# Performance work log

Measured on AMD Instinct MI355X. Metric: run time of the kernel, lower is better.

## Reference

```python
import jax, jax.numpy as jnp
import numpy as np

NUM_FEAT = 1024
NUM_GROUP = 16
DIM_K = NUM_FEAT // NUM_GROUP  # 64
FEAT_DIM = 64
WAVE_LENGTH = 1000.0


def position_embedding(box, ctx_box):
    # box: (M,4), ctx_box: (N,4) corner encoding -> (M*N, 64)
    xmin, ymin, xmax, ymax = jnp.split(box, 4, axis=1)            # (M,1) each
    bw = xmax - xmin + 1.0
    bh = ymax - ymin + 1.0
    cx = 0.5 * (xmin + xmax)
    cy = 0.5 * (ymin + ymax)
    cxmin, cymin, cxmax, cymax = jnp.split(ctx_box, 4, axis=1)    # (N,1) each
    cbw = cxmax - cxmin + 1.0
    cbh = cymax - cymin + 1.0
    ccx = 0.5 * (cxmin + cxmax)
    ccy = 0.5 * (cymin + cymax)
    dx = jnp.log(jnp.clip(jnp.abs((cx - ccx.T) / bw), 1e-3))      # (M,N)
    dy = jnp.log(jnp.clip(jnp.abs((cy - ccy.T) / bh), 1e-3))
    dw = jnp.log(cbw.T / bw)
    dh = jnp.log(cbh.T / bh)
    pos = jnp.stack((dx, dy, dw, dh), axis=2)                     # (M,N,4)
    feat_range = jnp.arange(FEAT_DIM // 8, dtype=jnp.float32)     # (8,)
    dim_mat = jnp.power(jnp.float32(WAVE_LENGTH), (8.0 / FEAT_DIM) * feat_range)
    div = (100.0 * pos)[..., None] / dim_mat                      # (M,N,4,8)
    emb = jnp.concatenate((jnp.sin(div), jnp.cos(div)), axis=3)   # (M,N,4,16)
    M, N = pos.shape[0], pos.shape[1]
    return emb.reshape(M * N, FEAT_DIM)


def setup_inputs() -> dict:
    key = jax.random.key(0)
    ks = jax.random.split(key, 12)
    M, N = 512, 1024

    def make_boxes(k, n):
        k1, k2 = jax.random.split(k)
        xy = jax.random.uniform(k1, (n, 2), dtype=jnp.float32) * 800.0
        wh = jax.random.uniform(k2, (n, 2), dtype=jnp.float32) * 200.0 + 1.0
        return jnp.concatenate([xy, xy + wh], axis=1)             # valid corners

    return {
        "feat": jax.random.normal(ks[0], (M, NUM_FEAT), dtype=jnp.float32),
        "ctx_feat": jax.random.normal(ks[1], (N, NUM_FEAT), dtype=jnp.float32),
        "box": make_boxes(ks[2], M),
        "ctx_box": make_boxes(ks[3], N),
        # torch Linear stores weight as (out, in); apply as x @ W.T + b
        "w_fc_gt": jax.random.normal(ks[4], (NUM_FEAT, 1024), dtype=jnp.float32) * 0.01,
        "b_fc_gt": jnp.zeros((NUM_FEAT,), dtype=jnp.float32),
        "w_fc_ctx": jax.random.normal(ks[5], (NUM_FEAT, 1024), dtype=jnp.float32) * 0.01,
        "b_fc_ctx": jnp.zeros((NUM_FEAT,), dtype=jnp.float32),
        "w_pos_gt": jax.random.normal(ks[6], (NUM_GROUP, FEAT_DIM), dtype=jnp.float32) * 0.01,
        "b_pos_gt": jnp.zeros((NUM_GROUP,), dtype=jnp.float32),
        "w_pos_ctx": jax.random.normal(ks[7], (NUM_GROUP, FEAT_DIM), dtype=jnp.float32) * 0.01,
        "b_pos_ctx": jnp.zeros((NUM_GROUP,), dtype=jnp.float32),
        # grouped 1x1 conv (16384 -> 1024, groups=16): per-group weight (64 out, 1024 in)
        "w_conv": jax.random.normal(ks[8], (NUM_GROUP, DIM_K, NUM_FEAT), dtype=jnp.float32) * 0.02,
        "b_conv": jnp.zeros((NUM_FEAT,), dtype=jnp.float32),
    }


def reference(feat, ctx_feat, box, ctx_box,
              w_fc_gt, b_fc_gt, w_fc_ctx, b_fc_ctx,
              w_pos_gt, b_pos_gt, w_pos_ctx, b_pos_ctx,
              w_conv, b_conv):
    M, N = feat.shape[0], ctx_feat.shape[0]
    # positional bias per group: (M*N,64) -relu-> linear -> (G,M,N)
    pe_gt = jax.nn.relu(position_embedding(box, ctx_box))
    pos_gt = (pe_gt @ w_pos_gt.T + b_pos_gt).T.reshape(NUM_GROUP, M, N)
    pe_ctx = jax.nn.relu(position_embedding(ctx_box, box))
    pos_ctx = (pe_ctx @ w_pos_ctx.T + b_pos_ctx).T.reshape(NUM_GROUP, N, M)
    # grouped projections
    q = (feat @ w_fc_gt.T + b_fc_gt).reshape(M, NUM_GROUP, DIM_K)
    k = (ctx_feat @ w_fc_ctx.T + b_fc_ctx).reshape(N, NUM_GROUP, DIM_K)
    scores = jnp.einsum('mgd,ngd->gmn', q, k) / np.float32(np.sqrt(DIM_K))  # (G,M,N)
    # gt <- ctx attention with log-position bias
    w1 = jax.nn.softmax(jnp.log(jnp.clip(pos_gt, 1e-6)) + scores, axis=-1)  # (G,M,N)
    att1 = jnp.einsum('gmn,nc->mgc', w1, ctx_feat)                          # (M,G,1024)
    out_gt = jnp.einsum('mgc,goc->mgo', att1, w_conv).reshape(M, NUM_FEAT) + b_conv
    # ctx <- gt attention (note: original module reuses gt_ctx_linear_out here)
    w2 = jax.nn.softmax(jnp.log(jnp.clip(pos_ctx, 1e-6)) + scores.transpose(0, 2, 1), axis=-1)  # (G,N,M)
    att2 = jnp.einsum('gnm,mc->ngc', w2, feat)                              # (N,G,1024)
    out_ctx = jnp.einsum('ngc,goc->ngo', att2, w_conv).reshape(N, NUM_FEAT) + b_conv
    return out_gt, out_ctx
```

## Files before the change

### kernel.cpp

```cpp
#include <hip/hip_runtime.h>
#include <math.h>


typedef __attribute__((ext_vector_type(8))) short short8;
typedef __attribute__((ext_vector_type(4))) float floatx4;
typedef __attribute__((ext_vector_type(4))) _Float16 half4;
typedef __attribute__((ext_vector_type(4))) unsigned uint4v;

__device__ inline unsigned short f32_bf16_rne(float x) {
    union { float f; unsigned u; } v; v.f = x;
    unsigned u = v.u;
    return (unsigned short)((u + 0x7fffu + ((u >> 16) & 1u)) >> 16);
}

__device__ inline unsigned fbits(float x) {
    union { float f; unsigned u; } v; v.f = x; return v.u;
}
__device__ inline float bitsf(unsigned u) {
    union { unsigned u; float f; } v; v.u = u; return v.f;
}
__device__ inline float h16f(unsigned short u) {
    union { unsigned short u; _Float16 h; } v; v.u = u; return (float)v.h;
}

__device__ __forceinline__ floatx4 mfma16(short8 a, short8 b, floatx4 c) {
    return __builtin_amdgcn_mfma_f32_16x16x32_bf16(a, b, c, 0, 0, 0);
}

__device__ __forceinline__ void gemm_tile_pack(
    const unsigned short* __restrict__ Ab, int lda,
    const unsigned short* __restrict__ Bb, int ldb, int K,
    unsigned short* __restrict__ out_base,
    const float* __restrict__ biasvec,
    unsigned short* As, unsigned short* Bs)
{
    const int tid = threadIdx.x;
    const int lr = tid >> 3;
    const int lk = (tid & 7) * 8;
    const int lane = tid & 63;
    const int wave = tid >> 6;
    const int qr = (wave >> 1) * 32;
    const int qc = (wave & 1) * 32;
    const int m = lane & 15;
    const int quad = lane >> 4;

    const unsigned short* Ap  = Ab + (long long)lr * lda + lk;
    const unsigned short* Ap2 = Ap + 32LL * lda;
    const unsigned short* Bp  = Bb + (long long)lr * ldb + lk;
    const unsigned short* Bp2 = Bp + 32LL * ldb;
    unsigned short* AsW  = As + lr * 72 + lk;
    unsigned short* AsW2 = As + (lr + 32) * 72 + lk;
    unsigned short* BsW  = Bs + lr * 72 + lk;
    unsigned short* BsW2 = Bs + (lr + 32) * 72 + lk;
    const unsigned short* a0p = As + (qr + m) * 72 + quad * 8;
    const unsigned short* b0p = Bs + (qc + m) * 72 + quad * 8;

    floatx4 acc00 = {0.f,0.f,0.f,0.f}, acc01 = {0.f,0.f,0.f,0.f};
    floatx4 acc10 = {0.f,0.f,0.f,0.f}, acc11 = {0.f,0.f,0.f,0.f};

    int4 pa0 = *(const int4*)Ap;
    int4 pa1 = *(const int4*)Ap2;
    int4 pb0 = *(const int4*)Bp;
    int4 pb1 = *(const int4*)Bp2;
    int4 qa0 = *(const int4*)(Ap + 64);
    int4 qa1 = *(const int4*)(Ap2 + 64);
    int4 qb0 = *(const int4*)(Bp + 64);
    int4 qb1 = *(const int4*)(Bp2 + 64);

    for (int k0 = 0; ; ) {
        __syncthreads();
        *(int4*)AsW  = pa0;
        *(int4*)AsW2 = pa1;
        *(int4*)BsW  = pb0;
        *(int4*)BsW2 = pb1;
        __syncthreads();
        pa0 = qa0; pa1 = qa1; pb0 = qb0; pb1 = qb1;
        const int kf = k0 + 128;
        if (kf < K) {
            qa0 = *(const int4*)(Ap + kf);
            qa1 = *(const int4*)(Ap2 + kf);
            qb0 = *(const int4*)(Bp + kf);
            qb1 = *(const int4*)(Bp2 + kf);
        }
        #pragma unroll
        for (int kk = 0; kk < 64; kk += 32) {
            short8 a0 = *(const short8*)(a0p + kk);
            short8 a1 = *(const short8*)(a0p + 16 * 72 + kk);
            short8 b0 = *(const short8*)(b0p + kk);
            short8 b1 = *(const short8*)(b0p + 16 * 72 + kk);
            acc00 = mfma16(a0, b0, acc00);
            acc01 = mfma16(a0, b1, acc01);
            acc10 = mfma16(a1, b0, acc10);
            acc11 = mfma16(a1, b1, acc11);
        }
        k0 += 64;
        if (k0 >= K) break;
    }

    float bias0 = 0.f, bias1 = 0.f;
    if (biasvec) { bias0 = biasvec[qc + m]; bias1 = biasvec[qc + 16 + m]; }

    __syncthreads();
    const floatx4 accs[2][2] = { {acc00, acc01}, {acc10, acc11} };
    #pragma unroll
    for (int i = 0; i < 2; ++i)
        #pragma unroll
        for (int r = 0; r < 4; ++r) {
            const int lrow = qr + i * 16 + quad * 4 + r;
            #pragma unroll
            for (int j = 0; j < 2; ++j) {
                const int lcol = qc + j * 16 + m;
                float val = accs[i][j][r] + (j ? bias1 : bias0);
                As[lrow * 72 + lcol] = f32_bf16_rne(val);
            }
        }
    __syncthreads();
    #pragma unroll
    for (int h = 0; h < 2; ++h) {
        const int f = h * 2048 + tid * 8;
        const int lanep = (f >> 3) & 63;
        const int part = (f >> 9) & 1;
        const int ploc = f >> 10;
        const int row = ploc * 16 + (lanep & 15);
        const int col = part * 32 + ((lanep >> 4) << 3);
        short8 v8 = *(const short8*)&As[row * 72 + col];
        *(short8*)(out_base + f) = v8;
    }
}

__global__ __launch_bounds__(256) void cast_kernel(
    const float* __restrict__ s0, unsigned short* __restrict__ d0,
    const float* __restrict__ s1, unsigned short* __restrict__ d1,
    const float* __restrict__ s2, unsigned short* __restrict__ d2,
    const float* __restrict__ s3, unsigned short* __restrict__ d3,
    const float* __restrict__ s4, unsigned short* __restrict__ d4)
{
    int bc = blockIdx.x;
    const float* s; unsigned short* d;
    if (bc < 512)       { s = s0; d = d0; }
    else if (bc < 1536) { s = s1; d = d1; bc -= 512; }
    else if (bc < 2560) { s = s2; d = d2; bc -= 1536; }
    else if (bc < 3584) { s = s3; d = d3; bc -= 2560; }
    else                { s = s4; d = d4; bc -= 3584; }
    const int idx = (bc * 256 + threadIdx.x) * 4;
    float4 v = *(const float4*)(s + idx);
    ushort4 o;
    o.x = f32_bf16_rne(v.x); o.y = f32_bf16_rne(v.y);
    o.z = f32_bf16_rne(v.z); o.w = f32_bf16_rne(v.w);
    *(ushort4*)(d + idx) = o;
}

__global__ __launch_bounds__(256) void posproj_kernel(
    const float* __restrict__ box, const float* __restrict__ ctx_box,
    const float* __restrict__ w_gt, const float* __restrict__ b_gt,
    const float* __restrict__ w_ctx, const float* __restrict__ b_ctx,
    _Float16* __restrict__ bias_gt, _Float16* __restrict__ bias_ctx,
    const unsigned short* __restrict__ in_bf, const unsigned short* __restrict__ wgt,
    const unsigned short* __restrict__ wctx,
    const float* __restrict__ bgt, const float* __restrict__ bctx,
    unsigned short* __restrict__ qk_pack,
    const unsigned short* __restrict__ wconv, unsigned short* __restrict__ vt_pack)
{
    __shared__ __align__(16) unsigned short smem[64 * 72 * 2];
    const int i = blockIdx.x;

    int pi;
    if (i < 4608) {
        const int k48 = i / 48;
        const int r48 = i - k48 * 48;
        if (r48 < 8) {
            const int j = r48;
            const int k = k48;
            const int g = j + 8 * (k & 1);
            const int rest = k >> 1;
            const int z = rest / 24;
            const int cc = rest - z * 24;
            unsigned short* As = smem;
            unsigned short* Bs = smem + 64 * 72;
            if (z == 0) {
                const int bm = cc * 64;
                const unsigned short* B = (bm < 512) ? wgt : wctx;
                const float* bias = (bm < 512) ? bgt : bctx;
                gemm_tile_pack(in_bf + (long long)bm * 1024, 1024,
                               B + (long long)g * 65536, 1024, 1024,
                               qk_pack + ((long long)g * 96 + cc * 4) * 1024,
                               bias + g * 64, As, Bs);
            } else {
                gemm_tile_pack(wconv + (long long)g * 65536, 1024,
                               in_bf + (long long)cc * 65536, 1024, 1024,
                               vt_pack + ((long long)g * 24 + cc) * 4096,
                               nullptr, As, Bs);
            }
            return;
        }
        pi = i - k48 * 8 - 8;
    } else {
        pi = i - 768;
    }

    const bool first = (pi < 2048);
    const long long blk = first ? pi : (pi - 2048);
    const float* boxA = first ? box : ctx_box;
    const float* boxB = first ? ctx_box : box;
    const float* w_pos = first ? w_gt : w_ctx;
    const float* b_pos = first ? b_gt : b_ctx;
    _Float16* out = first ? bias_gt : bias_ctx;
    const int shift = first ? 10 : 9;

    unsigned short* BsH = smem;
    unsigned short* BsL = smem + 16 * 72;
    float* posL = (float*)(smem + 32 * 72);
    _Float16* stg = (_Float16*)(posL + 4 * 68);

    const int tid = threadIdx.x;

    {
        const int g = tid >> 4;
        const int d = (tid & 15) * 4;
        float4 wv = *(const float4*)(w_pos + g * 64 + d);
        unsigned u0 = fbits(wv.x), u1 = fbits(wv.y);
        unsigned u2 = fbits(wv.z), u3 = fbits(wv.w);
        unsigned r0 = fbits(wv.x - bitsf(u0 & 0xFFFF0000u));
        unsigned r1 = fbits(wv.y - bitsf(u1 & 0xFFFF0000u));
        unsigned r2 = fbits(wv.z - bitsf(u2 & 0xFFFF0000u));
        unsigned r3 = fbits(wv.w - bitsf(u3 & 0xFFFF0000u));
        uint2 hv, lv;
        hv.x = (u0 >> 16) | (u1 & 0xFFFF0000u);
        hv.y = (u2 >> 16) | (u3 & 0xFFFF0000u);
        lv.x = (r0 >> 16) | (r1 & 0xFFFF0000u);
        lv.y = (r2 >> 16) | (r3 & 0xFFFF0000u);
        *(uint2*)&BsH[g * 72 + d] = hv;
        *(uint2*)&BsL[g * 72 + d] = lv;
    }
    __syncthreads();

    const int lane = tid & 63;
    const int w = tid >> 6;
    const int m = lane & 15;
    const int quad = lane >> 4;
    const bool qlow = (quad < 2);
    const float phase = (quad & 1) ? 1.57079632679f : 0.0f;
    const float bpv = b_pos[m];

    const unsigned short* bpH = &BsH[m * 72 + quad * 8];
    const unsigned short* bpL = &BsL[m * 72 + quad * 8];
    short8 bH0 = *(const short8*)bpH;
    short8 bH1 = *(const short8*)(bpH + 32);
    short8 bL0 = *(const short8*)bpL;
    short8 bL1 = *(const short8*)(bpL + 32);

    const float w100[8] = {100.f, 42.169650342f, 17.782794100f, 7.498942093f,
                           3.162277660f, 1.333521432f, 0.562341325f, 0.237137371f};
    const long long pbase = blk * 256;

    for (int it = 0; it < 4; ++it) {
        const long long pb = pbase + it * 64;

        {
            const int pl = tid & 63;
            const int p = tid >> 6;
            const long long pair = pb + pl;
            const int i2 = (int)(pair >> shift);
            const int j2 = (int)(pair & ((1 << shift) - 1));
            float4 ba = *(const float4*)(boxA + i2 * 4);
            float4 bb = *(const float4*)(boxB + j2 * 4);
            float posv;
            if (p == 0) {
                float r = __builtin_amdgcn_rcpf(ba.z - ba.x + 1.f);
                posv = __logf(fmaxf(fabsf((0.5f*(ba.x+ba.z) - 0.5f*(bb.x+bb.z)) * r), 1e-3f));
            } else if (p == 1) {
                float r = __builtin_amdgcn_rcpf(ba.w - ba.y + 1.f);
                posv = __logf(fmaxf(fabsf((0.5f*(ba.y+ba.w) - 0.5f*(bb.y+bb.w)) * r), 1e-3f));
            } else if (p == 2) {
                float r = __builtin_amdgcn_rcpf(ba.z - ba.x + 1.f);
                posv = __logf((bb.z - bb.x + 1.f) * r);
            } else {
                float r = __builtin_amdgcn_rcpf(ba.w - ba.y + 1.f);
                posv = __logf((bb.w - bb.y + 1.f) * r);
            }
            posL[p * 68 + pl] = posv;
        }
        __syncthreads();

        const int plB = w * 16 + m;
        const float pos_lo = posL[(qlow ? 0 : 1) * 68 + plB];
        const float pos_hi = posL[(qlow ? 2 : 3) * 68 + plB];

        unsigned hp0[4], lp0[4], hp1[4], lp1[4];
        #pragma unroll
        for (int fi = 0; fi < 4; ++fi) {
            float x0 = fmaxf(__sinf(fmaf(w100[2*fi],     pos_lo, phase)), 0.f);
            float x1 = fmaxf(__sinf(fmaf(w100[2*fi + 1], pos_lo, phase)), 0.f);
            unsigned u0 = fbits(x0), u1 = fbits(x1);
            unsigned r0 = fbits(x0 - bitsf(u0 & 0xFFFF0000u));
            unsigned r1 = fbits(x1 - bitsf(u1 & 0xFFFF0000u));
            hp0[fi] = (u0 >> 16) | (u1 & 0xFFFF0000u);
            lp0[fi] = (r0 >> 16) | (r1 & 0xFFFF0000u);
            float y0 = fmaxf(__sinf(fmaf(w100[2*fi],     pos_hi, phase)), 0.f);
            float y1 = fmaxf(__sinf(fmaf(w100[2*fi + 1], pos_hi, phase)), 0.f);
            unsigned v0 = fbits(y0), v1 = fbits(y1);
            unsigned s0r = fbits(y0 - bitsf(v0 & 0xFFFF0000u));
            unsigned s1r = fbits(y1 - bitsf(v1 & 0xFFFF0000u));
            hp1[fi] = (v0 >> 16) | (v1 & 0xFFFF0000u);
            lp1[fi] = (s0r >> 16) | (s1r & 0xFFFF0000u);
        }
        union { uint4v u; short8 s; } cH0, cL0, cH1, cL1;
        cH0.u = (uint4v){hp0[0], hp0[1], hp0[2], hp0[3]};
        cL0.u = (uint4v){lp0[0], lp0[1], lp0[2], lp0[3]};
        cH1.u = (uint4v){hp1[0], hp1[1], hp1[2], hp1[3]};
        cL1.u = (uint4v){lp1[0], lp1[1], lp1[2], lp1[3]};

        floatx4 acc = {0.f, 0.f, 0.f, 0.f};
        acc = mfma16(cH0.s, bH0, acc);
        acc = mfma16(cH1.s, bH1, acc);
        acc = mfma16(cH0.s, bL0, acc);
        acc = mfma16(cH1.s, bL1, acc);
        acc = mfma16(cL0.s, bH0, acc);
        acc = mfma16(cL1.s, bH1, acc);

        #pragma unroll
        for (int r = 0; r < 4; ++r)
            stg[m * 68 + w * 16 + quad * 4 + r] =
                (_Float16)fmaxf(acc[r] + bpv, 1e-6f);
        __syncthreads();

        const int g2 = tid >> 4, c16 = tid & 15;
        *(half4*)(out + (long long)g2 * 524288 + pb + c16 * 4) =
            *(const half4*)&stg[g2 * 68 + c16 * 4];
    }
}

template <int NC>
__device__ __forceinline__ void attn_body(
    int g, int bx,
    const unsigned short* __restrict__ qk, int pA, int pB0,
    const _Float16* __restrict__ bias,
    const unsigned short* __restrict__ vt, int cc0,
    const float* __restrict__ b_conv, float* __restrict__ outp,
    unsigned short* wpack, float* redB)
{
    constexpr int NCOL = NC * 64;
    constexpr int WS = NCOL + 8;
    constexpr int SHIFT = (NC == 16) ? 10 : 9;

    const int bm = bx * 16;
    const int tid = threadIdx.x;
    const int lane = tid & 63;
    const int w = tid >> 6;
    const int m = lane & 15;
    const int quad = lane >> 4;

    {
        const _Float16* bsrc = bias + (long long)g * 524288 + (long long)bm * NCOL;
        _Float16* bb = (_Float16*)wpack;
        #pragma unroll
        for (int i = 0; i < (16 * NCOL) / (256 * 8); ++i) {
            const int idx = (i * 256 + tid) * 8;
            const int row = idx >> SHIFT;
            const int col = idx & (NCOL - 1);
            *(int4*)(bb + row * WS + col) = *(const int4*)(bsrc + idx);
        }
    }

    const unsigned short* abase = qk + ((long long)(g * 96 + pA)) * 1024;
    short8 aq0 = *(const short8*)(abase + lane * 8);
    short8 aq1 = *(const short8*)(abase + 512 + lane * 8);

    const unsigned short* bptr = qk + ((long long)(g * 96 + pB0 + w)) * 1024 + lane * 8;
    short8 B0[2], B1[2];
    B0[0] = *(const short8*)bptr;
    B1[0] = *(const short8*)(bptr + 512);
    B0[1] = *(const short8*)(bptr + 4096);
    B1[1] = *(const short8*)(bptr + 4096 + 512);

    __syncthreads();

    float v[NC][4];
    #pragma unroll
    for (int c = 0; c < NC; ++c) {
        floatx4 acc = {0.f, 0.f, 0.f, 0.f};
        acc = mfma16(aq0, B0[c & 1], acc);
        acc = mfma16(aq1, B1[c & 1], acc);
        if (c + 2 < NC) {
            const unsigned short* nb = bptr + (long long)(c + 2) * 4096;
            B0[c & 1] = *(const short8*)nb;
            B1[c & 1] = *(const short8*)(nb + 512);
        }
        #pragma unroll
        for (int r = 0; r < 4; ++r)
            v[c][r] = acc[r];
    }

    const unsigned short* vptr = vt + ((long long)(g * 24 + cc0)) * 4096
                               + w * 1024 + lane * 8;
    short8 V0[2], V1[2];
    V0[0] = *(const short8*)vptr;
    V1[0] = *(const short8*)(vptr + 512);
    V0[1] = *(const short8*)(vptr + 4096);
    V1[1] = *(const short8*)(vptr + 4096 + 512);

    const int slot0 = (quad * 4) * WS + w * 16 + m;
    float rsum[4] = {0.f, 0.f, 0.f, 0.f};
    #pragma unroll
    for (int c = 0; c < NC; ++c)
        #pragma unroll
        for (int r = 0; r < 4; ++r) {
            const int a = slot0 + r * WS + c * 64;
            float p = h16f(wpack[a]);
            float e = exp2f(v[c][r] * 0.18033688f) * p;
            rsum[r] += e;
            wpack[a] = f32_bf16_rne(e);
        }
    #pragma unroll
    for (int r = 0; r < 4; ++r)
        #pragma unroll
        for (int off = 1; off < 16; off <<= 1)
            rsum[r] += __shfl_xor(rsum[r], off, 64);
    if (m == 0) {
        #pragma unroll
        for (int r = 0; r < 4; ++r) redB[w * 16 + quad * 4 + r] = rsum[r];
    }
    __syncthreads();

    float rinv[4];
    #pragma unroll
    for (int r = 0; r < 4; ++r)
        rinv[r] = 1.f / (redB[quad*4+r] + redB[16 + quad*4+r] +
                         redB[32 + quad*4+r] + redB[48 + quad*4+r]);

    floatx4 oacc = {0.f, 0.f, 0.f, 0.f};
    const unsigned short* awp = wpack + m * WS + quad * 8;
    #pragma unroll
    for (int kc = 0; kc < NC; ++kc) {
        short8 a0 = *(const short8*)(awp + kc * 64);
        short8 a1 = *(const short8*)(awp + kc * 64 + 32);
        oacc = mfma16(a0, V0[kc & 1], oacc);
        oacc = mfma16(a1, V1[kc & 1], oacc);
        if (kc + 2 < NC) {
            const unsigned short* nv = vptr + (long long)(kc + 2) * 4096;
            V0[kc & 1] = *(const short8*)nv;
            V1[kc & 1] = *(const short8*)(nv + 512);
        }
    }

    const int o = w * 16 + m;
    const float bc = b_conv[g * 64 + o];
    __syncthreads();
    float* ot = (float*)wpack;
    #pragma unroll
    for (int r = 0; r < 4; ++r)
        ot[(quad * 4 + r) * 68 + o] = fmaf(oacc[r], rinv[r], bc);
    __syncthreads();
    const int orow = tid >> 4, oc4 = (tid & 15) * 4;
    float4 ov = *(const float4*)&ot[orow * 68 + oc4];
    *(float4*)(outp + (long long)(bm + orow) * 1024 + g * 64 + oc4) = ov;
}

__global__ __launch_bounds__(256) void attn_out_kernel(
    const unsigned short* __restrict__ qk_pack,
    const _Float16* __restrict__ bias_gt, const _Float16* __restrict__ bias_ctx,
    const unsigned short* __restrict__ vt_pack, const float* __restrict__ b_conv,
    float* __restrict__ out_gt, float* __restrict__ out_ctx)
{
    __shared__ __align__(16) unsigned short wpack[16 * 1032];
    __shared__ float redB[64];

    const int bx = blockIdx.x;
    if (bx < 512) {
        const int g = bx & 15;
        const int rb = bx >> 4;
        attn_body<16>(g, rb, qk_pack, rb, 32,
                      bias_gt, vt_pack, 8, b_conv, out_gt,
                      wpack, redB);
    } else {
        const int b2 = bx - 512;
        const int g = b2 & 15;
        const int rb = b2 >> 4;
        attn_body<8>(g, rb, qk_pack, 32 + rb, 0,
                     bias_ctx, vt_pack, 0, b_conv, out_ctx,
                     wpack, redB);
    }
}

extern "C" void kernel_launch(void* const* d_in, const int* in_sizes, int n_in,
                              void* d_out, int out_size, void* d_ws, size_t ws_size,
                              hipStream_t stream)
{
    const float* feat     = (const float*)d_in[0];
    const float* ctx_feat = (const float*)d_in[1];
    const float* box      = (const float*)d_in[2];
    const float* ctx_box  = (const float*)d_in[3];
    const float* w_fc_gt  = (const float*)d_in[4];
    const float* b_fc_gt  = (const float*)d_in[5];
    const float* w_fc_ctx = (const float*)d_in[6];
    const float* b_fc_ctx = (const float*)d_in[7];
    const float* w_pos_gt = (const float*)d_in[8];
    const float* b_pos_gt = (const float*)d_in[9];
    const float* w_pos_ctx= (const float*)d_in[10];
    const float* b_pos_ctx= (const float*)d_in[11];
    const float* w_conv   = (const float*)d_in[12];
    const float* b_conv   = (const float*)d_in[13];

    float* ws = (float*)d_ws;
    unsigned short* in_bf   = (unsigned short*)ws;
    unsigned short* ctx_bf  = in_bf + 524288LL;
    unsigned short* qk_pack = in_bf + 1572864LL;
    _Float16* bias_gt  = (_Float16*)(ws + 1572864LL);
    _Float16* bias_ctx = (_Float16*)(ws + 5767168LL);
    unsigned short* wconv_bf = (unsigned short*)(ws + 9961472LL);
    unsigned short* vt_pack  = (unsigned short*)(ws + 10485760LL);
    unsigned short* wfcgt_bf = (unsigned short*)(ws + 11272192LL);
    unsigned short* wfcctx_bf= wfcgt_bf + 1048576LL;

    float* out_gt  = (float*)d_out;
    float* out_ctx = (float*)d_out + 524288LL;

    hipLaunchKernelGGL(cast_kernel, dim3(4608), dim3(256), 0, stream,
                       feat, in_bf,
                       ctx_feat, ctx_bf,
                       w_fc_gt, wfcgt_bf,
                       w_fc_ctx, wfcctx_bf,
                       w_conv, wconv_bf);

    hipLaunchKernelGGL(posproj_kernel, dim3(4864), dim3(256), 0, stream,
                       box, ctx_box, w_pos_gt, b_pos_gt, w_pos_ctx, b_pos_ctx,
                       bias_gt, bias_ctx,
                       in_bf, wfcgt_bf, wfcctx_bf, b_fc_gt, b_fc_ctx, qk_pack,
                       wconv_bf, vt_pack);

    hipLaunchKernelGGL(attn_out_kernel, dim3(1536), dim3(256), 0, stream,
                       qk_pack, bias_gt, bias_ctx, vt_pack, b_conv, out_gt, out_ctx);
}
```

Measured before the change: 147.6 us.

## Compute position features in registers and double attention rows per block

The position-projection kernel now computes each lane's position values directly from box coordinates, dropping the shared-memory staging and one barrier per iteration. Its output staging buffer is double-buffered across iterations. The attention kernel moves to 512-thread blocks covering 32 rows, with two row-groups of waves sharing the bias tile loads and V fragments. The exp/softmax weighting is fused into the score loop so the per-column scores no longer sit in a large register array. In exchange the blocks use more LDS and there are half as many of them, which may reduce occupancy.

Measured after the change: 147.4 us. Within noise of the previous version (-0.1%).

```diff
diff --git a/kernel.cpp b/kernel.cpp
--- a/kernel.cpp
+++ b/kernel.cpp
@@ -209,8 +209,7 @@
 
     unsigned short* BsH = smem;
     unsigned short* BsL = smem + 16 * 72;
-    float* posL = (float*)(smem + 32 * 72);
-    _Float16* stg = (_Float16*)(posL + 4 * 68);
+    _Float16* stg = (_Float16*)(smem + 32 * 72);
 
     const int tid = threadIdx.x;
 
@@ -241,6 +240,7 @@
     const bool qlow = (quad < 2);
     const float phase = (quad & 1) ? 1.57079632679f : 0.0f;
     const float bpv = b_pos[m];
+    const int plB = w * 16 + m;
 
     const unsigned short* bpH = &BsH[m * 72 + quad * 8];
     const unsigned short* bpL = &BsL[m * 72 + quad * 8];
@@ -256,35 +256,16 @@
     for (int it = 0; it < 4; ++it) {
         const long long pb = pbase + it * 64;
 
-        {
-            const int pl = tid & 63;
-            const int p = tid >> 6;
-            const long long pair = pb + pl;
-            const int i2 = (int)(pair >> shift);
-            const int j2 = (int)(pair & ((1 << shift) - 1));
-            float4 ba = *(const float4*)(boxA + i2 * 4);
-            float4 bb = *(const float4*)(boxB + j2 * 4);
-            float posv;
-            if (p == 0) {
-                float r = __builtin_amdgcn_rcpf(ba.z - ba.x + 1.f);
-                posv = __logf(fmaxf(fabsf((0.5f*(ba.x+ba.z) - 0.5f*(bb.x+bb.z)) * r), 1e-3f));
-            } else if (p == 1) {
-                float r = __builtin_amdgcn_rcpf(ba.w - ba.y + 1.f);
-                posv = __logf(fmaxf(fabsf((0.5f*(ba.y+ba.w) - 0.5f*(bb.y+bb.w)) * r), 1e-3f));
-            } else if (p == 2) {
-                float r = __builtin_amdgcn_rcpf(ba.z - ba.x + 1.f);
-                posv = __logf((bb.z - bb.x + 1.f) * r);
-            } else {
-                float r = __builtin_amdgcn_rcpf(ba.w - ba.y + 1.f);
-                posv = __logf((bb.w - bb.y + 1.f) * r);
-            }
-            posL[p * 68 + pl] = posv;
-        }
-        __syncthreads();
-
-        const int plB = w * 16 + m;
-        const float pos_lo = posL[(qlow ? 0 : 1) * 68 + plB];
-        const float pos_hi = posL[(qlow ? 2 : 3) * 68 + plB];
+        const int i2 = (int)(pb >> shift);
+        const int j2 = (int)(pb & ((1 << shift) - 1)) + plB;
+        float4 ba = *(const float4*)(boxA + i2 * 4);
+        float4 bb = *(const float4*)(boxB + j2 * 4);
+        const float a0 = qlow ? ba.x : ba.y, a1 = qlow ? ba.z : ba.w;
+        const float b0 = qlow ? bb.x : bb.y, b1 = qlow ? bb.z : bb.w;
+        const float rr = __builtin_amdgcn_rcpf(a1 - a0 + 1.f);
+        const float pos_lo =
+            __logf(fmaxf(fabsf((0.5f*(a0+a1) - 0.5f*(b0+b1)) * rr), 1e-3f));
+        const float pos_hi = __logf((b1 - b0 + 1.f) * rr);
 
         unsigned hp0[4], lp0[4], hp1[4], lp1[4];
         #pragma unroll
@@ -318,22 +299,23 @@
         acc = mfma16(cL0.s, bH0, acc);
         acc = mfma16(cL1.s, bH1, acc);
 
+        _Float16* s = stg + (it & 1) * 1088;
         #pragma unroll
         for (int r = 0; r < 4; ++r)
-            stg[m * 68 + w * 16 + quad * 4 + r] =
+            s[m * 68 + w * 16 + quad * 4 + r] =
                 (_Float16)fmaxf(acc[r] + bpv, 1e-6f);
         __syncthreads();
 
         const int g2 = tid >> 4, c16 = tid & 15;
         *(half4*)(out + (long long)g2 * 524288 + pb + c16 * 4) =
-            *(const half4*)&stg[g2 * 68 + c16 * 4];
+            *(const half4*)&s[g2 * 68 + c16 * 4];
     }
 }
 
 template <int NC>
 __device__ __forceinline__ void attn_body(
-    int g, int bx,
-    const unsigned short* __restrict__ qk, int pA, int pB0,
+    int g, int bm,
+    const unsigned short* __restrict__ qk, int pA0, int pB0,
     const _Float16* __restrict__ bias,
     const unsigned short* __restrict__ vt, int cc0,
     const float* __restrict__ b_conv, float* __restrict__ outp,
@@ -342,11 +324,13 @@
     constexpr int NCOL = NC * 64;
     constexpr int WS = NCOL + 8;
     constexpr int SHIFT = (NC == 16) ? 10 : 9;
-
-    const int bm = bx * 16;
+    constexpr int NSTG = (32 * NCOL) / (512 * 8);
+
     const int tid = threadIdx.x;
     const int lane = tid & 63;
     const int w = tid >> 6;
+    const int ws = w >> 2;
+    const int wq = w & 3;
     const int m = lane & 15;
     const int quad = lane >> 4;
 
@@ -354,19 +338,19 @@
         const _Float16* bsrc = bias + (long long)g * 524288 + (long long)bm * NCOL;
         _Float16* bb = (_Float16*)wpack;
         #pragma unroll
-        for (int i = 0; i < (16 * NCOL) / (256 * 8); ++i) {
-            const int idx = (i * 256 + tid) * 8;
+        for (int i = 0; i < NSTG; ++i) {
+            const int idx = (i * 512 + tid) * 8;
             const int row = idx >> SHIFT;
             const int col = idx & (NCOL - 1);
             *(int4*)(bb + row * WS + col) = *(const int4*)(bsrc + idx);
         }
     }
 
-    const unsigned short* abase = qk + ((long long)(g * 96 + pA)) * 1024;
+    const unsigned short* abase = qk + ((long long)(g * 96 + pA0 + ws)) * 1024;
     short8 aq0 = *(const short8*)(abase + lane * 8);
     short8 aq1 = *(const short8*)(abase + 512 + lane * 8);
 
-    const unsigned short* bptr = qk + ((long long)(g * 96 + pB0 + w)) * 1024 + lane * 8;
+    const unsigned short* bptr = qk + ((long long)(g * 96 + pB0 + wq)) * 1024 + lane * 8;
     short8 B0[2], B1[2];
     B0[0] = *(const short8*)bptr;
     B1[0] = *(const short8*)(bptr + 512);
@@ -375,7 +359,8 @@
 
     __syncthreads();
 
-    float v[NC][4];
+    const int slot0 = (ws * 16 + quad * 4) * WS + wq * 16 + m;
+    float rsum[4] = {0.f, 0.f, 0.f, 0.f};
     #pragma unroll
     for (int c = 0; c < NC; ++c) {
         floatx4 acc = {0.f, 0.f, 0.f, 0.f};
@@ -387,30 +372,23 @@
             B1[c & 1] = *(const short8*)(nb + 512);
         }
         #pragma unroll
-        for (int r = 0; r < 4; ++r)
-            v[c][r] = acc[r];
+        for (int r = 0; r < 4; ++r) {
+            const int a = slot0 + r * WS + c * 64;
+            float p = h16f(wpack[a]);
+            float e = exp2f(acc[r] * 0.18033688f) * p;
+            rsum[r] += e;
+            wpack[a] = f32_bf16_rne(e);
+        }
     }
 
     const unsigned short* vptr = vt + ((long long)(g * 24 + cc0)) * 4096
-                               + w * 1024 + lane * 8;
+                               + wq * 1024 + lane * 8;
     short8 V0[2], V1[2];
     V0[0] = *(const short8*)vptr;
     V1[0] = *(const short8*)(vptr + 512);
     V0[1] = *(const short8*)(vptr + 4096);
     V1[1] = *(const short8*)(vptr + 4096 + 512);
 
-    const int slot0 = (quad * 4) * WS + w * 16 + m;
-    float rsum[4] = {0.f, 0.f, 0.f, 0.f};
-    #pragma unroll
-    for (int c = 0; c < NC; ++c)
-        #pragma unroll
-        for (int r = 0; r < 4; ++r) {
-            const int a = slot0 + r * WS + c * 64;
-            float p = h16f(wpack[a]);
-            float e = exp2f(v[c][r] * 0.18033688f) * p;
-            rsum[r] += e;
-            wpack[a] = f32_bf16_rne(e);
-        }
     #pragma unroll
     for (int r = 0; r < 4; ++r)
         #pragma unroll
@@ -425,11 +403,11 @@
     float rinv[4];
     #pragma unroll
     for (int r = 0; r < 4; ++r)
-        rinv[r] = 1.f / (redB[quad*4+r] + redB[16 + quad*4+r] +
-                         redB[32 + quad*4+r] + redB[48 + quad*4+r]);
+        rinv[r] = 1.f / (redB[ws*64 + quad*4+r] + redB[ws*64 + 16 + quad*4+r] +
+                         redB[ws*64 + 32 + quad*4+r] + redB[ws*64 + 48 + quad*4+r]);
 
     floatx4 oacc = {0.f, 0.f, 0.f, 0.f};
-    const unsigned short* awp = wpack + m * WS + quad * 8;
+    const unsigned short* awp = wpack + (ws * 16 + m) * WS + quad * 8;
     #pragma unroll
     for (int kc = 0; kc < NC; ++kc) {
         short8 a0 = *(const short8*)(awp + kc * 64);
@@ -443,40 +421,40 @@
         }
     }
 
-    const int o = w * 16 + m;
+    const int o = wq * 16 + m;
     const float bc = b_conv[g * 64 + o];
     __syncthreads();
     float* ot = (float*)wpack;
     #pragma unroll
     for (int r = 0; r < 4; ++r)
-        ot[(quad * 4 + r) * 68 + o] = fmaf(oacc[r], rinv[r], bc);
+        ot[(ws * 16 + quad * 4 + r) * 68 + o] = fmaf(oacc[r], rinv[r], bc);
     __syncthreads();
     const int orow = tid >> 4, oc4 = (tid & 15) * 4;
     float4 ov = *(const float4*)&ot[orow * 68 + oc4];
     *(float4*)(outp + (long long)(bm + orow) * 1024 + g * 64 + oc4) = ov;
 }
 
-__global__ __launch_bounds__(256) void attn_out_kernel(
+__global__ __launch_bounds__(512) void attn_out_kernel(
     const unsigned short* __restrict__ qk_pack,
     const _Float16* __restrict__ bias_gt, const _Float16* __restrict__ bias_ctx,
     const unsigned short* __restrict__ vt_pack, const float* __restrict__ b_conv,
     float* __restrict__ out_gt, float* __restrict__ out_ctx)
 {
-    __shared__ __align__(16) unsigned short wpack[16 * 1032];
-    __shared__ float redB[64];
+    __shared__ __align__(16) unsigned short wpack[32 * 1032];
+    __shared__ float redB[128];
 
     const int bx = blockIdx.x;
-    if (bx < 512) {
+    if (bx < 256) {
         const int g = bx & 15;
         const int rb = bx >> 4;
-        attn_body<16>(g, rb, qk_pack, rb, 32,
+        attn_body<16>(g, rb * 32, qk_pack, 2 * rb, 32,
                       bias_gt, vt_pack, 8, b_conv, out_gt,
                       wpack, redB);
     } else {
-        const int b2 = bx - 512;
+        const int b2 = bx - 256;
         const int g = b2 & 15;
         const int rb = b2 >> 4;
-        attn_body<8>(g, rb, qk_pack, 32 + rb, 0,
+        attn_body<8>(g, rb * 32, qk_pack, 32 + 2 * rb, 0,
                      bias_ctx, vt_pack, 0, b_conv, out_ctx,
                      wpack, redB);
     }
@@ -528,6 +506,6 @@
                        in_bf, wfcgt_bf, wfcctx_bf, b_fc_gt, b_fc_ctx, qk_pack,
                        wconv_bf, vt_pack);
 
-    hipLaunchKernelGGL(attn_out_kernel, dim3(1536), dim3(256), 0, stream,
+    hipLaunchKernelGGL(attn_out_kernel, dim3(768), dim3(512), 0, stream,
                        qk_pack, bias_gt, bias_ctx, vt_pack, b_conv, out_gt, out_ctx);
 }
```
